# Kernel tuning notes

Measured on AMD Instinct MI355X. Metric: run time of the kernel, lower is better.

The kernel has to match this reference:

```python
import jax, jax.numpy as jnp
import numpy as np

B, T, C, H = 16, 4096, 256, 256

def setup_inputs() -> dict:
    key = jax.random.key(0)
    kx, kwi, kbi, kwh, kbh = jax.random.split(key, 5)
    s = 1.0 / np.sqrt(C)
    return {
        "x": jax.random.normal(kx, (B, T, C), dtype=jnp.float32),
        "Wi": jax.random.uniform(kwi, (H, C), dtype=jnp.float32, minval=-s, maxval=s),
        "bi": jax.random.uniform(kbi, (H,), dtype=jnp.float32, minval=-s, maxval=s),
        "Wh": jax.random.uniform(kwh, (H, H), dtype=jnp.float32, minval=-s, maxval=s),
        "bh": jax.random.uniform(kbh, (H,), dtype=jnp.float32, minval=-s, maxval=s),
    }

def reference(x, Wi, bi, Wh, bh):
    # Faithful to the source: Cell computes tanh(i2h(x) + h2h(x)) -- both
    # linears applied to x_t, the hidden state is never consumed, so there
    # is no recurrence and all timesteps can be computed in one fused pass.
    # hidden_states: [B, T, H]
    hidden_states = jnp.tanh(
        jnp.einsum("btc,hc->bth", x, Wi) + bi
        + jnp.einsum("btc,hc->bth", x, Wh) + bh
    )
    h_last = hidden_states[:, -1, :]  # h after the loop
    return (hidden_states, h_last)
```

## Files before the change

kernel.cpp:

```cpp
#include <hip/hip_runtime.h>


using short8 = __attribute__((ext_vector_type(8))) short;
using f32x4  = __attribute__((ext_vector_type(4))) float;

constexpr int Bn = 16, Tn = 4096, Cn = 256, Hn = 256;
constexpr int Mn = Bn * Tn;
constexpr int BM = 32;
constexpr int NBLK = Mn / BM;

__device__ inline unsigned pack2_bf16(float a, float b) {
  unsigned ua = __float_as_uint(a);
  unsigned ub = __float_as_uint(b);
  ua += 0x7fffu + ((ua >> 16) & 1u);
  ub += 0x7fffu + ((ub >> 16) & 1u);
  return (ua >> 16) | (ub & 0xffff0000u);
}

__global__ __launch_bounds__(256) void prep_kernel(
    const float* __restrict__ Wi, const float* __restrict__ bi,
    const float* __restrict__ Wh, const float* __restrict__ bh,
    unsigned short* __restrict__ Wc, float* __restrict__ bc) {
  int idx = blockIdx.x * 256 + threadIdx.x;
  float w = Wi[idx] + Wh[idx];
  unsigned u = __float_as_uint(w);
  u += 0x7fffu + ((u >> 16) & 1u);
  Wc[idx] = (unsigned short)(u >> 16);
  if (blockIdx.x == 0) bc[threadIdx.x] = bi[threadIdx.x] + bh[threadIdx.x];
}

__global__ __launch_bounds__(512, 4) void gemm_tanh_kernel(
    const float* __restrict__ x, const unsigned short* __restrict__ Wc,
    const float* __restrict__ bc, float* __restrict__ out) {
  __shared__ __align__(16) unsigned short Asm[BM * Cn];

  const int tid  = threadIdx.x;
  const int lane = tid & 63;
  const int wave = tid >> 6;
  const int rid  = lane & 15;
  const int kgrp = lane >> 4;
  const int m0   = blockIdx.x * BM;

  const int sr = tid >> 4;
  const int p  = tid & 15;
  const float4* src = (const float4*)(x + (size_t)(m0 + sr) * Cn) + 2 * p;
  float4 a0 = src[0];
  float4 a1 = src[1];
  float4 b0 = src[32];
  float4 b1 = src[33];

  short8 bf[2][8];
#pragma unroll
  for (int nt = 0; nt < 2; nt++) {
    int col = wave * 32 + nt * 16 + rid;
#pragma unroll
    for (int ks = 0; ks < 8; ks++)
      bf[nt][ks] = *(const short8*)&Wc[col * Cn + ks * 32 + kgrp * 8];
  }
  float bias[2];
  bias[0] = bc[wave * 32 + rid];
  bias[1] = bc[wave * 32 + 16 + rid];

  {
    const int s = sr & 7;
    uint4 P0, P1;
    P0.x = pack2_bf16(a0.x, a0.y);
    P0.y = pack2_bf16(a0.z, a0.w);
    P0.z = pack2_bf16(a1.x, a1.y);
    P0.w = pack2_bf16(a1.z, a1.w);
    P1.x = pack2_bf16(b0.x, b0.y);
    P1.y = pack2_bf16(b0.z, b0.w);
    P1.z = pack2_bf16(b1.x, b1.y);
    P1.w = pack2_bf16(b1.z, b1.w);
    *(uint4*)&Asm[sr * Cn + ((p ^ s) << 3)] = P0;
    *(uint4*)&Asm[sr * Cn + (((p + 16) ^ s) << 3)] = P1;
  }
  __syncthreads();

  f32x4 acc[2][2];
#pragma unroll
  for (int mt = 0; mt < 2; mt++)
#pragma unroll
    for (int nt = 0; nt < 2; nt++) acc[mt][nt] = (f32x4)0.f;

#pragma unroll
  for (int ks = 0; ks < 8; ks++) {
#pragma unroll
    for (int mt = 0; mt < 2; mt++) {
      int row = mt * 16 + rid;
      short8 a = *(const short8*)
          &Asm[row * Cn + ((((ks << 2) | kgrp) ^ (rid & 7)) << 3)];
#pragma unroll
      for (int nt = 0; nt < 2; nt++)
        acc[mt][nt] = __builtin_amdgcn_mfma_f32_16x16x32_bf16(
            a, bf[nt][ks], acc[mt][nt], 0, 0, 0);
    }
  }

#pragma unroll
  for (int nt = 0; nt < 2; nt++) {
    int n = wave * 32 + nt * 16 + rid;
#pragma unroll
    for (int mt = 0; mt < 2; mt++) {
#pragma unroll
      for (int r = 0; r < 4; r++) {
        int m   = m0 + mt * 16 + kgrp * 4 + r;
        float v = acc[mt][nt][r] + bias[nt];
        float tv = 1.f - 2.f / (__expf(2.f * v) + 1.f);
        out[(size_t)m * Hn + n] = tv;
        if ((m & (Tn - 1)) == (Tn - 1))
          out[(size_t)Mn * Hn + (size_t)(m >> 12) * Hn + n] = tv;
      }
    }
  }
}

extern "C" void kernel_launch(void* const* d_in, const int* in_sizes, int n_in,
                              void* d_out, int out_size, void* d_ws,
                              size_t ws_size, hipStream_t stream) {
  (void)in_sizes; (void)n_in; (void)out_size; (void)ws_size;
  const float* x  = (const float*)d_in[0];
  const float* Wi = (const float*)d_in[1];
  const float* bi = (const float*)d_in[2];
  const float* Wh = (const float*)d_in[3];
  const float* bh = (const float*)d_in[4];
  float* out = (float*)d_out;

  unsigned short* Wc = (unsigned short*)d_ws;
  float* bc = (float*)((char*)d_ws + (size_t)Hn * Cn * sizeof(unsigned short));

  prep_kernel<<<(Hn * Cn) / 256, 256, 0, stream>>>(Wi, bi, Wh, bh, Wc, bc);
  gemm_tanh_kernel<<<NBLK, 512, 0, stream>>>(x, Wc, bc, out);
}
```

Baseline: 143.8 us.

## Process four M-tiles per block with double-buffered LDS and register prefetch

Each block now handles four 32-row tiles instead of one. The B fragments (combined weights) are loaded once per block and reused across all four tiles. Global loads of x for tile t+2 are issued into registers while tile t computes, and tile t+1 is converted to bf16 into the alternate LDS buffer so loads overlap MFMA and the epilogue. The aim is to amortize the weight loads and hide x-load latency, at the cost of a quarter as many blocks, doubled LDS use, more registers and a hand-written barrier.

```diff
diff --git a/kernel.cpp b/kernel.cpp
--- a/kernel.cpp
+++ b/kernel.cpp
@@ -5,9 +5,12 @@
 using f32x4  = __attribute__((ext_vector_type(4))) float;
 
 constexpr int Bn = 16, Tn = 4096, Cn = 256, Hn = 256;
-constexpr int Mn = Bn * Tn;
-constexpr int BM = 32;
-constexpr int NBLK = Mn / BM;
+constexpr int Mn   = Bn * Tn;
+constexpr int BM   = 32;
+constexpr int TPB  = 4;
+constexpr int NBLK = Mn / (BM * TPB);
+
+#define PIPE_BARRIER() asm volatile("s_waitcnt lgkmcnt(0)\n\ts_barrier" ::: "memory")
 
 __device__ inline unsigned pack2_bf16(float a, float b) {
   unsigned ua = __float_as_uint(a);
@@ -32,22 +35,29 @@
 __global__ __launch_bounds__(512, 4) void gemm_tanh_kernel(
     const float* __restrict__ x, const unsigned short* __restrict__ Wc,
     const float* __restrict__ bc, float* __restrict__ out) {
-  __shared__ __align__(16) unsigned short Asm[BM * Cn];
+  __shared__ __align__(16) unsigned short Asm[2][BM * Cn];
 
   const int tid  = threadIdx.x;
   const int lane = tid & 63;
   const int wave = tid >> 6;
   const int rid  = lane & 15;
   const int kgrp = lane >> 4;
-  const int m0   = blockIdx.x * BM;
+  const int mBase = blockIdx.x * (BM * TPB);
 
   const int sr = tid >> 4;
   const int p  = tid & 15;
-  const float4* src = (const float4*)(x + (size_t)(m0 + sr) * Cn) + 2 * p;
-  float4 a0 = src[0];
-  float4 a1 = src[1];
-  float4 b0 = src[32];
-  float4 b1 = src[33];
+  const int s  = sr & 7;
+
+  float4 xr[2][4];
+#pragma unroll
+  for (int t = 0; t < 2; t++) {
+    const float4* src =
+        (const float4*)(x + (size_t)(mBase + t * BM + sr) * Cn) + 2 * p;
+    xr[t][0] = src[0];
+    xr[t][1] = src[1];
+    xr[t][2] = src[32];
+    xr[t][3] = src[33];
+  }
 
   short8 bf[2][8];
 #pragma unroll
@@ -62,56 +72,86 @@
   bias[1] = bc[wave * 32 + 16 + rid];
 
   {
-    const int s = sr & 7;
     uint4 P0, P1;
-    P0.x = pack2_bf16(a0.x, a0.y);
-    P0.y = pack2_bf16(a0.z, a0.w);
-    P0.z = pack2_bf16(a1.x, a1.y);
-    P0.w = pack2_bf16(a1.z, a1.w);
-    P1.x = pack2_bf16(b0.x, b0.y);
-    P1.y = pack2_bf16(b0.z, b0.w);
-    P1.z = pack2_bf16(b1.x, b1.y);
-    P1.w = pack2_bf16(b1.z, b1.w);
-    *(uint4*)&Asm[sr * Cn + ((p ^ s) << 3)] = P0;
-    *(uint4*)&Asm[sr * Cn + (((p + 16) ^ s) << 3)] = P1;
+    P0.x = pack2_bf16(xr[0][0].x, xr[0][0].y);
+    P0.y = pack2_bf16(xr[0][0].z, xr[0][0].w);
+    P0.z = pack2_bf16(xr[0][1].x, xr[0][1].y);
+    P0.w = pack2_bf16(xr[0][1].z, xr[0][1].w);
+    P1.x = pack2_bf16(xr[0][2].x, xr[0][2].y);
+    P1.y = pack2_bf16(xr[0][2].z, xr[0][2].w);
+    P1.z = pack2_bf16(xr[0][3].x, xr[0][3].y);
+    P1.w = pack2_bf16(xr[0][3].z, xr[0][3].w);
+    *(uint4*)&Asm[0][sr * Cn + ((p ^ s) << 3)] = P0;
+    *(uint4*)&Asm[0][sr * Cn + (((p + 16) ^ s) << 3)] = P1;
   }
-  __syncthreads();
-
-  f32x4 acc[2][2];
-#pragma unroll
-  for (int mt = 0; mt < 2; mt++)
-#pragma unroll
-    for (int nt = 0; nt < 2; nt++) acc[mt][nt] = (f32x4)0.f;
+  PIPE_BARRIER();
 
 #pragma unroll
-  for (int ks = 0; ks < 8; ks++) {
+  for (int t = 0; t < TPB; t++) {
+    const int cur = t & 1;
+
+    if (t + 2 < TPB) {
+      const float4* src =
+          (const float4*)(x + (size_t)(mBase + (t + 2) * BM + sr) * Cn) + 2 * p;
+      xr[cur][0] = src[0];
+      xr[cur][1] = src[1];
+      xr[cur][2] = src[32];
+      xr[cur][3] = src[33];
+    }
+
+    f32x4 acc[2][2];
 #pragma unroll
-    for (int mt = 0; mt < 2; mt++) {
-      int row = mt * 16 + rid;
-      short8 a = *(const short8*)
-          &Asm[row * Cn + ((((ks << 2) | kgrp) ^ (rid & 7)) << 3)];
+    for (int mt = 0; mt < 2; mt++)
 #pragma unroll
-      for (int nt = 0; nt < 2; nt++)
-        acc[mt][nt] = __builtin_amdgcn_mfma_f32_16x16x32_bf16(
-            a, bf[nt][ks], acc[mt][nt], 0, 0, 0);
-    }
-  }
+      for (int nt = 0; nt < 2; nt++) acc[mt][nt] = (f32x4)0.f;
 
 #pragma unroll
-  for (int nt = 0; nt < 2; nt++) {
-    int n = wave * 32 + nt * 16 + rid;
+    for (int ks = 0; ks < 8; ks++) {
 #pragma unroll
-    for (int mt = 0; mt < 2; mt++) {
+      for (int mt = 0; mt < 2; mt++) {
+        int row = mt * 16 + rid;
+        short8 a = *(const short8*)
+            &Asm[cur][row * Cn + ((((ks << 2) | kgrp) ^ (rid & 7)) << 3)];
 #pragma unroll
-      for (int r = 0; r < 4; r++) {
-        int m   = m0 + mt * 16 + kgrp * 4 + r;
-        float v = acc[mt][nt][r] + bias[nt];
-        float tv = 1.f - 2.f / (__expf(2.f * v) + 1.f);
-        out[(size_t)m * Hn + n] = tv;
-        if ((m & (Tn - 1)) == (Tn - 1))
-          out[(size_t)Mn * Hn + (size_t)(m >> 12) * Hn + n] = tv;
+        for (int nt = 0; nt < 2; nt++)
+          acc[mt][nt] = __builtin_amdgcn_mfma_f32_16x16x32_bf16(
+              a, bf[nt][ks], acc[mt][nt], 0, 0, 0);
       }
     }
+
+    if (t + 1 < TPB) {
+      const float4* r = xr[cur ^ 1];
+      uint4 P0, P1;
+      P0.x = pack2_bf16(r[0].x, r[0].y);
+      P0.y = pack2_bf16(r[0].z, r[0].w);
+      P0.z = pack2_bf16(r[1].x, r[1].y);
+      P0.w = pack2_bf16(r[1].z, r[1].w);
+      P1.x = pack2_bf16(r[2].x, r[2].y);
+      P1.y = pack2_bf16(r[2].z, r[2].w);
+      P1.z = pack2_bf16(r[3].x, r[3].y);
+      P1.w = pack2_bf16(r[3].z, r[3].w);
+      *(uint4*)&Asm[cur ^ 1][sr * Cn + ((p ^ s) << 3)] = P0;
+      *(uint4*)&Asm[cur ^ 1][sr * Cn + (((p + 16) ^ s) << 3)] = P1;
+    }
+
+#pragma unroll
+    for (int nt = 0; nt < 2; nt++) {
+      int n = wave * 32 + nt * 16 + rid;
+#pragma unroll
+      for (int mt = 0; mt < 2; mt++) {
+#pragma unroll
+        for (int r = 0; r < 4; r++) {
+          int m   = mBase + t * BM + mt * 16 + kgrp * 4 + r;
+          float v = acc[mt][nt][r] + bias[nt];
+          float tv = 1.f - 2.f / (__expf(2.f * v) + 1.f);
+          out[(size_t)m * Hn + n] = tv;
+          if ((m & (Tn - 1)) == (Tn - 1))
+            out[(size_t)Mn * Hn + (size_t)(m >> 12) * Hn + n] = tv;
+        }
+      }
+    }
+
+    if (t + 1 < TPB) PIPE_BARRIER();
   }
 }
 
```

New measurement: 131.0 us. 1.1x faster.
